# Kernel optimization log

Hardware: AMD Instinct MI355X
Metric: run time of the kernel (lower is better)

## Reference

```python
import jax, jax.numpy as jnp
import numpy as np

D_MODEL = 1024
N_HEADS = 16
D_HEAD = D_MODEL // N_HEADS
B, T = 4, 2048


def setup_inputs() -> dict:
    key = jax.random.key(0)
    ks = jax.random.split(key, 5)
    s = 1.0 / np.sqrt(D_MODEL)
    x = jax.random.normal(ks[0], (B, T, D_MODEL), dtype=jnp.float32)
    Wq = jax.random.uniform(ks[1], (D_MODEL, D_MODEL), jnp.float32, -s, s)
    Wk = jax.random.uniform(ks[2], (D_MODEL, D_MODEL), jnp.float32, -s, s)
    Wv = jax.random.uniform(ks[3], (D_MODEL, D_MODEL), jnp.float32, -s, s)
    Wo = jax.random.uniform(ks[4], (D_MODEL, D_MODEL), jnp.float32, -s, s)
    # causal mask, 0 = masked (matches torch masked_fill(mask == 0, -inf))
    mask = jnp.tril(jnp.ones((T, T), dtype=jnp.int32))[None, None, :, :]
    return {"x": x, "Wq": Wq, "Wk": Wk, "Wv": Wv, "Wo": Wo, "mask": mask}


def reference(x, Wq, Wk, Wv, Wo, mask):
    def split_heads(t):  # [B,T,D] -> [B,H,T,d]
        return t.reshape(B, T, N_HEADS, D_HEAD).transpose(0, 2, 1, 3)

    Q = split_heads(x @ Wq.T)
    K = split_heads(x @ Wk.T)
    V = split_heads(x @ Wv.T)
    scale = 1.0 / np.sqrt(D_HEAD).astype(np.float32)
    attn = jnp.einsum('bhqd,bhkd->bhqk', Q, K) * scale
    attn = jnp.where(mask == 0, -jnp.inf, attn)
    attn = jax.nn.softmax(attn, axis=-1)
    out = jnp.einsum('bhqk,bhkd->bhqd', attn, V)
    out = out.transpose(0, 2, 1, 3).reshape(B, T, D_MODEL)
    return out @ Wo.T
```

## Files before the change

kernel.cpp:

```cpp
#include <hip/hip_runtime.h>
#include <hip/hip_bf16.h>
#include <cstdint>

#define T_SEQ   2048
#define DMODEL  1024
#define NHEADS  16
#define DHEAD   64
#define B_SZ    4
#define M_ROWS  (B_SZ * T_SEQ)

typedef unsigned short u16;
typedef __attribute__((ext_vector_type(8))) __bf16 bf16x8;
typedef __attribute__((ext_vector_type(4))) float  f32x4;

__device__ __forceinline__ u16 f2bf(float f) {
  uint32_t u = __float_as_uint(f);
  u += 0x7FFF + ((u >> 16) & 1);
  return (u16)(u >> 16);
}

__device__ __forceinline__ void gload_lds16(const void* g, void* l) {
  __builtin_amdgcn_global_load_lds(
      (const __attribute__((address_space(1))) void*)g,
      (__attribute__((address_space(3))) void*)l, 16, 0, 0);
}

__global__ void cvt_f32_bf16(const float* __restrict__ src, u16* __restrict__ dst, int n8) {
  int i = blockIdx.x * blockDim.x + threadIdx.x;
  int stride = gridDim.x * blockDim.x;
  for (; i < n8; i += stride) {
    const float4* s = (const float4*)src;
    float4 a = s[2 * i], b = s[2 * i + 1];
    union { u16 u[8]; uint4 v; } o;
    o.u[0] = f2bf(a.x); o.u[1] = f2bf(a.y); o.u[2] = f2bf(a.z); o.u[3] = f2bf(a.w);
    o.u[4] = f2bf(b.x); o.u[5] = f2bf(b.y); o.u[6] = f2bf(b.z); o.u[7] = f2bf(b.w);
    ((uint4*)dst)[i] = o.v;
  }
}

template <int MODE>
__global__ __launch_bounds__(256) void gemm_bt(
    const u16* __restrict__ A, const u16* __restrict__ W,
    void* __restrict__ Cp, float scale) {
  constexpr int K = DMODEL, N = DMODEL;
  __shared__ u16 As[128 * 64];
  __shared__ u16 Bs[128 * 64];
  const int tid = threadIdx.x;
  const int wid = tid >> 6, lane = tid & 63;
  const int tm = blockIdx.x >> 3, tn = blockIdx.x & 7;
  const int wr = wid >> 1, wc = wid & 1;
  const int lrow = lane & 15, lq = lane >> 4;
  const int srow = lane >> 3, scol = (lane & 7) * 8;

  f32x4 acc[4][4];
#pragma unroll
  for (int m = 0; m < 4; m++)
#pragma unroll
    for (int n = 0; n < 4; n++) acc[m][n] = f32x4{0.f, 0.f, 0.f, 0.f};

  for (int k0 = 0; k0 < K; k0 += 64) {
#pragma unroll
    for (int it = 0; it < 4; ++it) {
      int rbase = it * 32 + wid * 8;
      gload_lds16(A + (size_t)(tm * 128 + rbase + srow) * K + k0 + scol, &As[rbase * 64]);
      gload_lds16(W + (size_t)(tn * 128 + rbase + srow) * K + k0 + scol, &Bs[rbase * 64]);
    }
    __syncthreads();
#pragma unroll
    for (int kk = 0; kk < 2; ++kk) {
      bf16x8 a[4], b[4];
      const int ko = kk * 32 + lq * 8;
#pragma unroll
      for (int m = 0; m < 4; m++) a[m] = *(const bf16x8*)&As[(wr * 64 + m * 16 + lrow) * 64 + ko];
#pragma unroll
      for (int n = 0; n < 4; n++) b[n] = *(const bf16x8*)&Bs[(wc * 64 + n * 16 + lrow) * 64 + ko];
#pragma unroll
      for (int m = 0; m < 4; m++)
#pragma unroll
        for (int n = 0; n < 4; n++)
          acc[m][n] = __builtin_amdgcn_mfma_f32_16x16x32_bf16(a[m], b[n], acc[m][n], 0, 0, 0);
    }
    __syncthreads();
  }

#pragma unroll
  for (int m = 0; m < 4; m++) {
#pragma unroll
    for (int n = 0; n < 4; n++) {
#pragma unroll
      for (int v = 0; v < 4; v++) {
        int i = tm * 128 + wr * 64 + m * 16 + lq * 4 + v;
        int j = tn * 128 + wc * 64 + n * 16 + lrow;
        float val = acc[m][n][v] * scale;
        if constexpr (MODE == 0) {
          ((float*)Cp)[(size_t)i * N + j] = val;
        } else if constexpr (MODE == 1) {
          int b_ = i >> 11, t_ = i & 2047, h_ = j >> 6, d_ = j & 63;
          ((u16*)Cp)[((size_t)(b_ * NHEADS + h_) * T_SEQ + t_) * 64 + d_] = f2bf(val);
        } else {
          int b_ = i >> 11, t_ = i & 2047, h_ = j >> 6, d_ = j & 63;
          ((u16*)Cp)[((size_t)(b_ * NHEADS + h_) * 64 + d_) * T_SEQ + t_] = f2bf(val);
        }
      }
    }
  }
}

__global__ __launch_bounds__(256) void flash_attn(
    const u16* __restrict__ Q, const u16* __restrict__ Kg,
    const u16* __restrict__ Vt, u16* __restrict__ Ao) {
  __shared__ u16 Ks[2][64 * 64];
  __shared__ u16 Vs[2][64 * 64];
  __shared__ u16 Ps[4][16 * 64];
  const int tid = threadIdx.x, wid = tid >> 6, lane = tid & 63;
  const int qi = blockIdx.x, bh = blockIdx.y;
  const int qtA = qi, qtB = 31 - qi;
  const int lrow = lane & 15, lq = lane >> 4;
  const int sr = lrow & 7;
  const int srow = lane >> 3;
  const int csw = ((lane & 7) ^ srow) * 8;

  const u16* qbase = Q + ((size_t)bh * T_SEQ + wid * 16 + lrow) * 64 + lq * 8;
  const bf16x8 qA0 = *(const bf16x8*)(qbase + (size_t)qtA * 4096);
  const bf16x8 qA1 = *(const bf16x8*)(qbase + (size_t)qtA * 4096 + 32);
  const bf16x8 qB0 = *(const bf16x8*)(qbase + (size_t)qtB * 4096);
  const bf16x8 qB1 = *(const bf16x8*)(qbase + (size_t)qtB * 4096 + 32);

  bf16x8 ones;
  {
    union { u16 u; __bf16 b; } c; c.u = 0x3F80;
#pragma unroll
    for (int j = 0; j < 8; j++) ones[j] = c.b;
  }

  f32x4 poA[4], poB[4], lA, lB;
#pragma unroll
  for (int n = 0; n < 4; n++) { poA[n] = f32x4{0.f,0.f,0.f,0.f}; poB[n] = f32x4{0.f,0.f,0.f,0.f}; }
  lA = f32x4{0.f,0.f,0.f,0.f}; lB = f32x4{0.f,0.f,0.f,0.f};

  auto stage = [&](int kt, int b) {
#pragma unroll
    for (int it = 0; it < 2; ++it) {
      int rbase = it * 32 + wid * 8;
      gload_lds16(Kg + ((size_t)bh * T_SEQ + kt * 64 + rbase + srow) * 64 + csw,
                  &Ks[b][rbase * 64]);
      gload_lds16(Vt + ((size_t)bh * 64 + rbase + srow) * T_SEQ + kt * 64 + csw,
                  &Vs[b][rbase * 64]);
    }
  };

  stage(0, 0);
  __syncthreads();
  int cur = 0;

  for (int kt = 0; kt <= qtB; ++kt) {
    if (kt < qtB) stage(kt + 1, cur ^ 1);

    bf16x8 kf0[4], kf1[4];
#pragma unroll
    for (int n = 0; n < 4; n++) {
      kf0[n] = *(const bf16x8*)&Ks[cur][(n * 16 + lrow) * 64 + ((lq ^ sr) * 8)];
      kf1[n] = *(const bf16x8*)&Ks[cur][(n * 16 + lrow) * 64 + (((lq + 4) ^ sr) * 8)];
    }

    auto apply = [&](const bf16x8& q0, const bf16x8& q1,
                     f32x4 (&po)[4], f32x4& l4, bool diag) {
      f32x4 s[4];
#pragma unroll
      for (int n = 0; n < 4; n++) {
        f32x4 a = f32x4{0.f, 0.f, 0.f, 0.f};
        a = __builtin_amdgcn_mfma_f32_16x16x32_bf16(q0, kf0[n], a, 0, 0, 0);
        a = __builtin_amdgcn_mfma_f32_16x16x32_bf16(q1, kf1[n], a, 0, 0, 0);
        s[n] = a;
      }
      if (diag) {
#pragma unroll
        for (int n = 0; n < 4; n++)
#pragma unroll
          for (int v = 0; v < 4; v++) {
            int kcol = n * 16 + lrow;
            int qrow = wid * 16 + lq * 4 + v;
            if (kcol > qrow) s[n][v] = -1e30f;
          }
      }
#pragma unroll
      for (int n = 0; n < 4; n++)
#pragma unroll
        for (int v = 0; v < 4; v++) {
          float p = __expf(s[n][v]);
          int col = n * 16 + lrow;
          int r = lq * 4 + v;
          Ps[wid][r * 64 + (((col >> 3) ^ (r & 7)) * 8) + (col & 7)] = f2bf(p);
        }
#pragma unroll
      for (int kk = 0; kk < 2; kk++) {
        bf16x8 pa = *(const bf16x8*)&Ps[wid][lrow * 64 + (((kk * 4 + lq) ^ sr) * 8)];
#pragma unroll
        for (int n = 0; n < 4; n++) {
          bf16x8 vf = *(const bf16x8*)&Vs[cur][(n * 16 + lrow) * 64 + (((kk * 4 + lq) ^ sr) * 8)];
          po[n] = __builtin_amdgcn_mfma_f32_16x16x32_bf16(pa, vf, po[n], 0, 0, 0);
        }
        l4 = __builtin_amdgcn_mfma_f32_16x16x32_bf16(pa, ones, l4, 0, 0, 0);
      }
    };

    if (kt <= qtA) apply(qA0, qA1, poA, lA, kt == qtA);
    apply(qB0, qB1, poB, lB, kt == qtB);

    asm volatile("s_waitcnt vmcnt(0)" ::: "memory");
    __syncthreads();
    cur ^= 1;
  }

  const int b_ = bh >> 4, h_ = bh & 15;
  auto epi = [&](int qt_, f32x4 (&po)[4], f32x4& l4) {
    float rl[4];
#pragma unroll
    for (int v = 0; v < 4; v++) rl[v] = 1.0f / l4[v];
#pragma unroll
    for (int n = 0; n < 4; n++)
#pragma unroll
      for (int v = 0; v < 4; v++) {
        int t_ = qt_ * 64 + wid * 16 + lq * 4 + v;
        int col = h_ * 64 + n * 16 + lrow;
        Ao[((size_t)b_ * T_SEQ + t_) * DMODEL + col] = f2bf(po[n][v] * rl[v]);
      }
  };
  epi(qtA, poA, lA);
  epi(qtB, poB, lB);
}

extern "C" void kernel_launch(void* const* d_in, const int* in_sizes, int n_in,
                              void* d_out, int out_size, void* d_ws, size_t ws_size,
                              hipStream_t stream) {
  const float* x  = (const float*)d_in[0];
  const float* Wq = (const float*)d_in[1];
  const float* Wk = (const float*)d_in[2];
  const float* Wv = (const float*)d_in[3];
  const float* Wo = (const float*)d_in[4];
  float* out = (float*)d_out;

  char* ws = (char*)d_ws;
  u16* xb  = (u16*)(ws);
  u16* Wb  = (u16*)(ws + 16777216);
  u16* Qb  = (u16*)(ws + 25165824);
  u16* Kb  = (u16*)(ws + 41943040);
  u16* Vtb = (u16*)(ws + 58720256);
  u16* Aob = xb;

  cvt_f32_bf16<<<4096, 256, 0, stream>>>(x, xb, (B_SZ * T_SEQ * DMODEL) / 8);
  cvt_f32_bf16<<<512, 256, 0, stream>>>(Wq, Wb + 0 * 1048576, (DMODEL * DMODEL) / 8);
  cvt_f32_bf16<<<512, 256, 0, stream>>>(Wk, Wb + 1 * 1048576, (DMODEL * DMODEL) / 8);
  cvt_f32_bf16<<<512, 256, 0, stream>>>(Wv, Wb + 2 * 1048576, (DMODEL * DMODEL) / 8);
  cvt_f32_bf16<<<512, 256, 0, stream>>>(Wo, Wb + 3 * 1048576, (DMODEL * DMODEL) / 8);

  const int gemm_grid = (M_ROWS / 128) * (DMODEL / 128);
  gemm_bt<1><<<gemm_grid, 256, 0, stream>>>(xb, Wb + 0 * 1048576, Qb, 0.125f);
  gemm_bt<1><<<gemm_grid, 256, 0, stream>>>(xb, Wb + 1 * 1048576, Kb, 1.0f);
  gemm_bt<2><<<gemm_grid, 256, 0, stream>>>(xb, Wb + 2 * 1048576, Vtb, 1.0f);

  flash_attn<<<dim3(16, B_SZ * NHEADS), 256, 0, stream>>>(Qb, Kb, Vtb, Aob);

  gemm_bt<0><<<gemm_grid, 256, 0, stream>>>(Aob, Wb + 3 * 1048576, out, 1.0f);
}
```

Measured before the change: 223.6 us.

## Fuse conversions and QKV GEMMs, double-buffer GEMM, remap blocks per XCD, use exp2

Result: faster. 198.9 us (-11.1%).

```diff
diff --git a/kernel.cpp b/kernel.cpp
--- a/kernel.cpp
+++ b/kernel.cpp
@@ -8,6 +8,7 @@
 #define DHEAD   64
 #define B_SZ    4
 #define M_ROWS  (B_SZ * T_SEQ)
+#define QSCALE  0.1803368801111204f
 
 typedef unsigned short u16;
 typedef __attribute__((ext_vector_type(8))) __bf16 bf16x8;
@@ -19,68 +20,106 @@
   return (u16)(u >> 16);
 }
 
+__device__ __forceinline__ float fast_exp2(float x) {
+  return __builtin_amdgcn_exp2f(x);
+}
+
 __device__ __forceinline__ void gload_lds16(const void* g, void* l) {
   __builtin_amdgcn_global_load_lds(
       (const __attribute__((address_space(1))) void*)g,
       (__attribute__((address_space(3))) void*)l, 16, 0, 0);
 }
 
-__global__ void cvt_f32_bf16(const float* __restrict__ src, u16* __restrict__ dst, int n8) {
+__global__ void cvt_all(const float* __restrict__ x,  const float* __restrict__ Wq,
+                        const float* __restrict__ Wk, const float* __restrict__ Wv,
+                        const float* __restrict__ Wo, u16* __restrict__ xb,
+                        u16* __restrict__ Wb) {
+  const int NX = (B_SZ * T_SEQ * DMODEL) / 8;
+  const int NW = (DMODEL * DMODEL) / 8;
   int i = blockIdx.x * blockDim.x + threadIdx.x;
   int stride = gridDim.x * blockDim.x;
-  for (; i < n8; i += stride) {
-    const float4* s = (const float4*)src;
-    float4 a = s[2 * i], b = s[2 * i + 1];
+  for (; i < NX + 4 * NW; i += stride) {
+    const float* src; u16* dst; int idx;
+    if (i < NX) { src = x; dst = xb; idx = i; }
+    else {
+      int j = i - NX, w = j >> 17;
+      idx = j & (NW - 1);
+      src = (w == 0) ? Wq : (w == 1) ? Wk : (w == 2) ? Wv : Wo;
+      dst = Wb + (size_t)w * (DMODEL * DMODEL);
+    }
+    const float4* s4 = (const float4*)src;
+    float4 a = s4[2 * idx], b = s4[2 * idx + 1];
     union { u16 u[8]; uint4 v; } o;
     o.u[0] = f2bf(a.x); o.u[1] = f2bf(a.y); o.u[2] = f2bf(a.z); o.u[3] = f2bf(a.w);
     o.u[4] = f2bf(b.x); o.u[5] = f2bf(b.y); o.u[6] = f2bf(b.z); o.u[7] = f2bf(b.w);
-    ((uint4*)dst)[i] = o.v;
+    ((uint4*)dst)[idx] = o.v;
   }
 }
 
 template <int MODE>
-__global__ __launch_bounds__(256) void gemm_bt(
-    const u16* __restrict__ A, const u16* __restrict__ W,
-    void* __restrict__ Cp, float scale) {
-  constexpr int K = DMODEL, N = DMODEL;
-  __shared__ u16 As[128 * 64];
-  __shared__ u16 Bs[128 * 64];
+__global__ __launch_bounds__(256) void gemm2(
+    const u16* __restrict__ A, const u16* __restrict__ Wall,
+    float* __restrict__ C0, u16* __restrict__ Qb, u16* __restrict__ Kb,
+    u16* __restrict__ Vtb) {
+  constexpr int K = DMODEL;
+  constexpr int NT = (MODE == 0) ? 8 : 24;
+  __shared__ u16 As[2][128 * 64];
+  __shared__ u16 Bs[2][128 * 64];
   const int tid = threadIdx.x;
   const int wid = tid >> 6, lane = tid & 63;
-  const int tm = blockIdx.x >> 3, tn = blockIdx.x & 7;
+  const int flat = blockIdx.x;
+  const int xcd = flat & 7, serial = flat >> 3;
+  const int tm = (serial / NT) * 8 + xcd;
+  const int tn = serial % NT;
   const int wr = wid >> 1, wc = wid & 1;
   const int lrow = lane & 15, lq = lane >> 4;
-  const int srow = lane >> 3, scol = (lane & 7) * 8;
-
-  f32x4 acc[4][4];
-#pragma unroll
-  for (int m = 0; m < 4; m++)
-#pragma unroll
-    for (int n = 0; n < 4; n++) acc[m][n] = f32x4{0.f, 0.f, 0.f, 0.f};
-
-  for (int k0 = 0; k0 < K; k0 += 64) {
+  const int sr = lrow & 7;
+  const int srow = lane >> 3;
+  const int csw = ((lane & 7) ^ srow) * 8;
+
+  const u16* Arow = A    + (size_t)(tm * 128 + srow) * K + csw;
+  const u16* Wrow = Wall + (size_t)(tn * 128 + srow) * K + csw;
+
+  auto stage = [&](int k0, int b) {
 #pragma unroll
     for (int it = 0; it < 4; ++it) {
       int rbase = it * 32 + wid * 8;
-      gload_lds16(A + (size_t)(tm * 128 + rbase + srow) * K + k0 + scol, &As[rbase * 64]);
-      gload_lds16(W + (size_t)(tn * 128 + rbase + srow) * K + k0 + scol, &Bs[rbase * 64]);
-    }
-    __syncthreads();
+      gload_lds16(Arow + (size_t)rbase * K + k0, &As[b][rbase * 64]);
+      gload_lds16(Wrow + (size_t)rbase * K + k0, &Bs[b][rbase * 64]);
+    }
+  };
+
+  f32x4 acc[4][4];
+#pragma unroll
+  for (int m = 0; m < 4; m++)
+#pragma unroll
+    for (int n = 0; n < 4; n++) acc[m][n] = f32x4{0.f, 0.f, 0.f, 0.f};
+
+  stage(0, 0);
+  __syncthreads();
+  int cur = 0;
+
+  for (int t = 0; t < K / 64; ++t) {
+    if (t < K / 64 - 1) stage((t + 1) * 64, cur ^ 1);
 #pragma unroll
     for (int kk = 0; kk < 2; ++kk) {
       bf16x8 a[4], b[4];
-      const int ko = kk * 32 + lq * 8;
-#pragma unroll
-      for (int m = 0; m < 4; m++) a[m] = *(const bf16x8*)&As[(wr * 64 + m * 16 + lrow) * 64 + ko];
-#pragma unroll
-      for (int n = 0; n < 4; n++) b[n] = *(const bf16x8*)&Bs[(wc * 64 + n * 16 + lrow) * 64 + ko];
+      const int co = ((kk * 4 + lq) ^ sr) * 8;
+#pragma unroll
+      for (int m = 0; m < 4; m++)
+        a[m] = *(const bf16x8*)&As[cur][(wr * 64 + m * 16 + lrow) * 64 + co];
+#pragma unroll
+      for (int n = 0; n < 4; n++)
+        b[n] = *(const bf16x8*)&Bs[cur][(wc * 64 + n * 16 + lrow) * 64 + co];
 #pragma unroll
       for (int m = 0; m < 4; m++)
 #pragma unroll
         for (int n = 0; n < 4; n++)
           acc[m][n] = __builtin_amdgcn_mfma_f32_16x16x32_bf16(a[m], b[n], acc[m][n], 0, 0, 0);
     }
+    asm volatile("s_waitcnt vmcnt(0)" ::: "memory");
     __syncthreads();
+    cur ^= 1;
   }
 
 #pragma unroll
@@ -91,15 +130,16 @@
       for (int v = 0; v < 4; v++) {
         int i = tm * 128 + wr * 64 + m * 16 + lq * 4 + v;
         int j = tn * 128 + wc * 64 + n * 16 + lrow;
-        float val = acc[m][n][v] * scale;
         if constexpr (MODE == 0) {
-          ((float*)Cp)[(size_t)i * N + j] = val;
-        } else if constexpr (MODE == 1) {
-          int b_ = i >> 11, t_ = i & 2047, h_ = j >> 6, d_ = j & 63;
-          ((u16*)Cp)[((size_t)(b_ * NHEADS + h_) * T_SEQ + t_) * 64 + d_] = f2bf(val);
+          C0[(size_t)i * DMODEL + j] = acc[m][n][v];
         } else {
-          int b_ = i >> 11, t_ = i & 2047, h_ = j >> 6, d_ = j & 63;
-          ((u16*)Cp)[((size_t)(b_ * NHEADS + h_) * 64 + d_) * T_SEQ + t_] = f2bf(val);
+          int y = j >> 10, jj = j & 1023;
+          float val = acc[m][n][v] * (y == 0 ? QSCALE : 1.0f);
+          int b_ = i >> 11, t_ = i & 2047, h_ = jj >> 6, d_ = jj & 63;
+          if (y == 2)
+            Vtb[((size_t)(b_ * NHEADS + h_) * 64 + d_) * T_SEQ + t_] = f2bf(val);
+          else
+            ((y == 0) ? Qb : Kb)[((size_t)(b_ * NHEADS + h_) * T_SEQ + t_) * 64 + d_] = f2bf(val);
         }
       }
     }
@@ -113,7 +153,10 @@
   __shared__ u16 Vs[2][64 * 64];
   __shared__ u16 Ps[4][16 * 64];
   const int tid = threadIdx.x, wid = tid >> 6, lane = tid & 63;
-  const int qi = blockIdx.x, bh = blockIdx.y;
+  const int flat = blockIdx.x;
+  const int serial = flat >> 3;
+  const int bh = (serial >> 4) * 8 + (flat & 7);
+  const int qi = serial & 15;
   const int qtA = qi, qtB = 31 - qi;
   const int lrow = lane & 15, lq = lane >> 4;
   const int sr = lrow & 7;
@@ -187,10 +230,11 @@
       for (int n = 0; n < 4; n++)
 #pragma unroll
         for (int v = 0; v < 4; v++) {
-          float p = __expf(s[n][v]);
+          float p = fast_exp2(s[n][v]);
           int col = n * 16 + lrow;
           int r = lq * 4 + v;
-          Ps[wid][r * 64 + (((col >> 3) ^ (r & 7)) * 8) + (col & 7)] = f2bf(p);
+          Ps[wid][r * 64 + (((col >> 3) ^ (r & 7)) * 8) + (col & 7)] =
+              (u16)(__float_as_uint(p) >> 16);
         }
 #pragma unroll
       for (int kk = 0; kk < 2; kk++) {
@@ -248,18 +292,11 @@
   u16* Vtb = (u16*)(ws + 58720256);
   u16* Aob = xb;
 
-  cvt_f32_bf16<<<4096, 256, 0, stream>>>(x, xb, (B_SZ * T_SEQ * DMODEL) / 8);
-  cvt_f32_bf16<<<512, 256, 0, stream>>>(Wq, Wb + 0 * 1048576, (DMODEL * DMODEL) / 8);
-  cvt_f32_bf16<<<512, 256, 0, stream>>>(Wk, Wb + 1 * 1048576, (DMODEL * DMODEL) / 8);
-  cvt_f32_bf16<<<512, 256, 0, stream>>>(Wv, Wb + 2 * 1048576, (DMODEL * DMODEL) / 8);
-  cvt_f32_bf16<<<512, 256, 0, stream>>>(Wo, Wb + 3 * 1048576, (DMODEL * DMODEL) / 8);
-
-  const int gemm_grid = (M_ROWS / 128) * (DMODEL / 128);
-  gemm_bt<1><<<gemm_grid, 256, 0, stream>>>(xb, Wb + 0 * 1048576, Qb, 0.125f);
-  gemm_bt<1><<<gemm_grid, 256, 0, stream>>>(xb, Wb + 1 * 1048576, Kb, 1.0f);
-  gemm_bt<2><<<gemm_grid, 256, 0, stream>>>(xb, Wb + 2 * 1048576, Vtb, 1.0f);
-
-  flash_attn<<<dim3(16, B_SZ * NHEADS), 256, 0, stream>>>(Qb, Kb, Vtb, Aob);
-
-  gemm_bt<0><<<gemm_grid, 256, 0, stream>>>(Aob, Wb + 3 * 1048576, out, 1.0f);
-}
+  cvt_all<<<2048, 256, 0, stream>>>(x, Wq, Wk, Wv, Wo, xb, Wb);
+
+  gemm2<1><<<1536, 256, 0, stream>>>(xb, Wb, nullptr, Qb, Kb, Vtb);
+
+  flash_attn<<<1024, 256, 0, stream>>>(Qb, Kb, Vtb, Aob);
+
+  gemm2<0><<<512, 256, 0, stream>>>(Aob, Wb + 3 * 1048576, out, nullptr, nullptr, nullptr);
+}
```
